# Kernel tuning notes

Measured on AMD Instinct MI355X. Metric: run time of the kernel, lower is better.

The kernel has to match this reference:

```python
import jax, jax.numpy as jnp
import numpy as np
from jax.scipy.special import logsumexp

B, D, T, O = 8, 64, 512, 256  # batch, channels (d_dim), observed timestamps, grid points


def setup_inputs() -> dict:
    key = jax.random.key(0)
    k1, k2, k3 = jax.random.split(key, 3)
    vals = jax.random.normal(k1, (B, D, T), dtype=jnp.float32)
    mask = (jax.random.uniform(k2, (B, D, T)) < 0.7).astype(jnp.float32)
    mask = mask.at[:, :, 0].set(1.0)  # ensure >=1 observation per (b, channel)
    times = jnp.sort(jax.random.uniform(k3, (B, D, T), dtype=jnp.float32), axis=-1)
    x = jnp.concatenate([vals, mask, times], axis=1)  # (B, 3*D, T)
    grid = jnp.broadcast_to(jnp.linspace(0.0, 1.0, O, dtype=jnp.float32), (B, O))
    kernel = jnp.zeros((D,), dtype=jnp.float32)  # learned per-channel log-bandwidth
    return {"x": x, "interpolation_grid": grid, "kernel": kernel}


def reference(x, interpolation_grid, kernel):
    d_dim = kernel.shape[0]
    x_t = x[:, :d_dim]            # (B, D, T) observed values
    m = x[:, d_dim:2 * d_dim]     # (B, D, T) observation mask in {0,1}
    t = x[:, 2 * d_dim:3 * d_dim] # (B, D, T) observation timestamps

    alpha = jax.nn.softplus(kernel)[None, :, None, None]  # pos_kernel, (1,D,1,1)
    # squared distance between observed times and reference grid: (B,D,T,O)
    norm = (t[:, :, :, None] - interpolation_grid[:, None, None, :]) ** 2
    # log(mask): -inf (clamped) where unobserved, 0 where observed
    logm = jnp.log(jnp.maximum(m, 1e-30))[:, :, :, None]

    s = -alpha * norm + logm                      # (B,D,T,O) masked RBF logits
    w = logsumexp(s, axis=2)                      # (B,D,O) intensity channel
    w1 = jnp.exp(s - w[:, :, None, :])            # softmax over T
    y = jnp.sum(w1 * x_t[:, :, :, None], axis=2)  # (B,D,O) smooth interpolation

    s10 = -10.0 * alpha * norm + logm             # sharper kernel (transient)
    wt_lse = logsumexp(s10, axis=2)
    wt = jnp.exp(s10 - wt_lse[:, :, None, :])
    y_trans = jnp.sum(wt * x_t[:, :, :, None], axis=2)  # (B,D,O)

    return jnp.concatenate([y, w, y_trans], axis=1)  # (B, 3*D, O)
```

## Files before the change

### kernel.cpp

```cpp
#include <hip/hip_runtime.h>
#include <math.h>


namespace {
constexpr int kB = 8, kD = 64, kT = 512, kO = 256;
constexpr float kLOG2E = 1.4426950408889634f;
constexpr float kLN2   = 0.6931471805599453f;
constexpr int kTH = 512;
}

__device__ __forceinline__ float rlane(float v, int l) {
    return __int_as_float(__builtin_amdgcn_readlane(__float_as_int(v), l));
}

__global__ __launch_bounds__(kTH, 4) void interp_kernel(
    const float* __restrict__ x,
    const float* __restrict__ grid,
    const float* __restrict__ kern,
    float* __restrict__ out)
{
    __shared__ float sp[4][4][kO];

    const int tid  = threadIdx.x;
    const int lane = tid & 63;
    const int wv   = tid >> 6;
    const int ow   = wv & 1;
    const int tw   = wv >> 1;
    const int o0   = ow * 128 + lane;
    const int t0   = tw * 128;

    const int bd = blockIdx.x;
    const int b  = bd >> 6;
    const int d  = bd & (kD - 1);

    const float* base = x + (size_t)b * (3 * kD * kT);
    const float* Vrow = base + (size_t)d * kT;
    const float* Mrow = base + (size_t)(kD + d) * kT;
    const float* Trow = base + (size_t)(2 * kD + d) * kT;

    const float k     = kern[d];
    const float alpha = fmaxf(k, 0.0f) + log1pf(expf(-fabsf(k)));
    const float a2    = alpha * kLOG2E;

    const float tt0 = Trow[t0 + lane],      tt1 = Trow[t0 + 64 + lane];
    const float mm0 = Mrow[t0 + lane],      mm1 = Mrow[t0 + 64 + lane];
    const float vv0 = Vrow[t0 + lane],      vv1 = Vrow[t0 + 64 + lane];
    const float lm0 = __builtin_amdgcn_logf(fmaxf(mm0, 1e-30f));
    const float lm1 = __builtin_amdgcn_logf(fmaxf(mm1, 1e-30f));
    const float u0  = fmaf(-a2 * tt0, tt0, lm0);
    const float u1  = fmaf(-a2 * tt1, tt1, lm1);
    const float w0  = 2.0f * a2 * tt0;
    const float w1  = 2.0f * a2 * tt1;

    const float g0 = grid[b * kO + o0];
    const float g1 = grid[b * kO + o0 + 64];

    float l_0=0.f,l_1=0.f, y_0=0.f,y_1=0.f, q_0=0.f,q_1=0.f, z_0=0.f,z_1=0.f;

    #pragma unroll
    for (int j = 0; j < 64; ++j) {
        { const float us = rlane(u0, j), ws = rlane(w0, j), vs = rlane(vv0, j);
          const float a0 = ws * g0 + us;
          const float a1 = ws * g1 + us;
          const float e0 = __builtin_amdgcn_exp2f(a0);
          const float E0 = __builtin_amdgcn_exp2f(10.0f * a0);
          const float e1 = __builtin_amdgcn_exp2f(a1);
          const float E1 = __builtin_amdgcn_exp2f(10.0f * a1);
          l_0 += e0; y_0 = fmaf(e0, vs, y_0); q_0 += E0; z_0 = fmaf(E0, vs, z_0);
          l_1 += e1; y_1 = fmaf(e1, vs, y_1); q_1 += E1; z_1 = fmaf(E1, vs, z_1); }
        { const float us = rlane(u1, j), ws = rlane(w1, j), vs = rlane(vv1, j);
          const float a0 = ws * g0 + us;
          const float a1 = ws * g1 + us;
          const float e0 = __builtin_amdgcn_exp2f(a0);
          const float E0 = __builtin_amdgcn_exp2f(10.0f * a0);
          const float e1 = __builtin_amdgcn_exp2f(a1);
          const float E1 = __builtin_amdgcn_exp2f(10.0f * a1);
          l_0 += e0; y_0 = fmaf(e0, vs, y_0); q_0 += E0; z_0 = fmaf(E0, vs, z_0);
          l_1 += e1; y_1 = fmaf(e1, vs, y_1); q_1 += E1; z_1 = fmaf(E1, vs, z_1); }
    }

    sp[tw][0][o0] = l_0;  sp[tw][0][o0 + 64] = l_1;
    sp[tw][1][o0] = y_0;  sp[tw][1][o0 + 64] = y_1;
    sp[tw][2][o0] = q_0;  sp[tw][2][o0 + 64] = q_1;
    sp[tw][3][o0] = z_0;  sp[tw][3][o0 + 64] = z_1;
    __syncthreads();

    if (tw == 0) {
        float L0=0.f,L1=0.f, Y0=0.f,Y1=0.f, Q0=0.f,Q1=0.f, Z0=0.f,Z1=0.f;
        #pragma unroll
        for (int j = 0; j < 4; ++j) {
            L0 += sp[j][0][o0]; Y0 += sp[j][1][o0];
            Q0 += sp[j][2][o0]; Z0 += sp[j][3][o0];
            L1 += sp[j][0][o0 + 64]; Y1 += sp[j][1][o0 + 64];
            Q1 += sp[j][2][o0 + 64]; Z1 += sp[j][3][o0 + 64];
        }
        const float c0 = -a2 * g0 * g0;
        const float c1 = -a2 * g1 * g1;
        const float w0o = (__builtin_amdgcn_logf(L0) + c0) * kLN2;
        const float w1o = (__builtin_amdgcn_logf(L1) + c1) * kLN2;
        float* ob = out + (size_t)b * (3 * kD * kO);
        ob[(size_t)d * kO + o0]                 = Y0 / L0;
        ob[(size_t)d * kO + o0 + 64]            = Y1 / L1;
        ob[(size_t)(kD + d) * kO + o0]          = w0o;
        ob[(size_t)(kD + d) * kO + o0 + 64]     = w1o;
        ob[(size_t)(2 * kD + d) * kO + o0]      = Z0 / Q0;
        ob[(size_t)(2 * kD + d) * kO + o0 + 64] = Z1 / Q1;
    }
}

extern "C" void kernel_launch(void* const* d_in, const int* in_sizes, int n_in,
                              void* d_out, int out_size, void* d_ws, size_t ws_size,
                              hipStream_t stream) {
    const float* x    = (const float*)d_in[0];
    const float* grid = (const float*)d_in[1];
    const float* kern = (const float*)d_in[2];
    float* out        = (float*)d_out;
    interp_kernel<<<dim3(kB * kD), dim3(kTH), 0, stream>>>(x, grid, kern, out);
}
```

Before: 80.14 us.

## Stage per-timestamp coefficients in LDS and fold grid constant into exponent

Precomputed u, w and v per timestamp now go into shared memory and are read back as float4 vectors, replacing the per-iteration readlane broadcasts from registers. The -a2*g^2 term moves inside the exponent, which adds one op per element and makes the exponent relative to the true RBF distance. The log of the mask becomes a linear map (mask*kLM - kLM), avoiding a log instruction but assuming the mask is exactly 0 or 1. LDS reads replace the SALU/readlane path, while the exp-bound inner loop is left unchanged.

```diff
diff --git a/kernel.cpp b/kernel.cpp
--- a/kernel.cpp
+++ b/kernel.cpp
@@ -4,13 +4,10 @@
 
 namespace {
 constexpr int kB = 8, kD = 64, kT = 512, kO = 256;
+constexpr int kTH = 512;
 constexpr float kLOG2E = 1.4426950408889634f;
 constexpr float kLN2   = 0.6931471805599453f;
-constexpr int kTH = 512;
-}
-
-__device__ __forceinline__ float rlane(float v, int l) {
-    return __int_as_float(__builtin_amdgcn_readlane(__float_as_int(v), l));
+constexpr float kLM    = 99.65784284662087f;
 }
 
 __global__ __launch_bounds__(kTH, 4) void interp_kernel(
@@ -19,15 +16,18 @@
     const float* __restrict__ kern,
     float* __restrict__ out)
 {
-    __shared__ float sp[4][4][kO];
+    __shared__ __align__(16) float smem[4096];
+    float* s_u = smem;
+    float* s_w = smem + kT;
+    float* s_v = smem + 2 * kT;
 
     const int tid  = threadIdx.x;
     const int lane = tid & 63;
     const int wv   = tid >> 6;
     const int ow   = wv & 1;
-    const int tw   = wv >> 1;
+    const int tq   = wv >> 1;
     const int o0   = ow * 128 + lane;
-    const int t0   = tw * 128;
+    const int o1   = o0 + 64;
 
     const int bd = blockIdx.x;
     const int b  = bd >> 6;
@@ -42,69 +42,70 @@
     const float alpha = fmaxf(k, 0.0f) + log1pf(expf(-fabsf(k)));
     const float a2    = alpha * kLOG2E;
 
-    const float tt0 = Trow[t0 + lane],      tt1 = Trow[t0 + 64 + lane];
-    const float mm0 = Mrow[t0 + lane],      mm1 = Mrow[t0 + 64 + lane];
-    const float vv0 = Vrow[t0 + lane],      vv1 = Vrow[t0 + 64 + lane];
-    const float lm0 = __builtin_amdgcn_logf(fmaxf(mm0, 1e-30f));
-    const float lm1 = __builtin_amdgcn_logf(fmaxf(mm1, 1e-30f));
-    const float u0  = fmaf(-a2 * tt0, tt0, lm0);
-    const float u1  = fmaf(-a2 * tt1, tt1, lm1);
-    const float w0  = 2.0f * a2 * tt0;
-    const float w1  = 2.0f * a2 * tt1;
+    {
+        const float tt = Trow[tid];
+        const float mm = Mrow[tid];
+        const float lm = fmaf(mm, kLM, -kLM);
+        s_u[tid] = fmaf(-a2 * tt, tt, lm);
+        s_w[tid] = 2.0f * a2 * tt;
+        s_v[tid] = Vrow[tid];
+    }
+    __syncthreads();
 
     const float g0 = grid[b * kO + o0];
-    const float g1 = grid[b * kO + o0 + 64];
+    const float g1 = grid[b * kO + o1];
+    const float c0 = -a2 * g0 * g0;
+    const float c1 = -a2 * g1 * g1;
 
     float l_0=0.f,l_1=0.f, y_0=0.f,y_1=0.f, q_0=0.f,q_1=0.f, z_0=0.f,z_1=0.f;
 
-    #pragma unroll
-    for (int j = 0; j < 64; ++j) {
-        { const float us = rlane(u0, j), ws = rlane(w0, j), vs = rlane(vv0, j);
-          const float a0 = ws * g0 + us;
-          const float a1 = ws * g1 + us;
-          const float e0 = __builtin_amdgcn_exp2f(a0);
-          const float E0 = __builtin_amdgcn_exp2f(10.0f * a0);
-          const float e1 = __builtin_amdgcn_exp2f(a1);
-          const float E1 = __builtin_amdgcn_exp2f(10.0f * a1);
-          l_0 += e0; y_0 = fmaf(e0, vs, y_0); q_0 += E0; z_0 = fmaf(E0, vs, z_0);
-          l_1 += e1; y_1 = fmaf(e1, vs, y_1); q_1 += E1; z_1 = fmaf(E1, vs, z_1); }
-        { const float us = rlane(u1, j), ws = rlane(w1, j), vs = rlane(vv1, j);
-          const float a0 = ws * g0 + us;
-          const float a1 = ws * g1 + us;
-          const float e0 = __builtin_amdgcn_exp2f(a0);
-          const float E0 = __builtin_amdgcn_exp2f(10.0f * a0);
-          const float e1 = __builtin_amdgcn_exp2f(a1);
-          const float E1 = __builtin_amdgcn_exp2f(10.0f * a1);
-          l_0 += e0; y_0 = fmaf(e0, vs, y_0); q_0 += E0; z_0 = fmaf(E0, vs, z_0);
-          l_1 += e1; y_1 = fmaf(e1, vs, y_1); q_1 += E1; z_1 = fmaf(E1, vs, z_1); }
+    const int t0 = tq * 128;
+    #pragma unroll 2
+    for (int t = t0; t < t0 + 128; t += 4) {
+        const float4 uu = *(const float4*)(s_u + t);
+        const float4 ww = *(const float4*)(s_w + t);
+        const float4 vv = *(const float4*)(s_v + t);
+
+        #pragma unroll
+        for (int j = 0; j < 4; ++j) {
+            const float u = (&uu.x)[j], w = (&ww.x)[j], v = (&vv.x)[j];
+            const float a0 = fmaf(w, g0, u) + c0;
+            const float a1 = fmaf(w, g1, u) + c1;
+            const float e0 = __builtin_amdgcn_exp2f(a0);
+            const float E0 = __builtin_amdgcn_exp2f(10.0f * a0);
+            const float e1 = __builtin_amdgcn_exp2f(a1);
+            const float E1 = __builtin_amdgcn_exp2f(10.0f * a1);
+            l_0 += e0; y_0 = fmaf(e0, v, y_0); q_0 += E0; z_0 = fmaf(E0, v, z_0);
+            l_1 += e1; y_1 = fmaf(e1, v, y_1); q_1 += E1; z_1 = fmaf(E1, v, z_1);
+        }
     }
 
-    sp[tw][0][o0] = l_0;  sp[tw][0][o0 + 64] = l_1;
-    sp[tw][1][o0] = y_0;  sp[tw][1][o0 + 64] = y_1;
-    sp[tw][2][o0] = q_0;  sp[tw][2][o0 + 64] = q_1;
-    sp[tw][3][o0] = z_0;  sp[tw][3][o0 + 64] = z_1;
+    __syncthreads();
+    float (*sp)[4][kO] = (float (*)[4][kO])smem;
+    sp[tq][0][o0] = l_0;  sp[tq][0][o1] = l_1;
+    sp[tq][1][o0] = y_0;  sp[tq][1][o1] = y_1;
+    sp[tq][2][o0] = q_0;  sp[tq][2][o1] = q_1;
+    sp[tq][3][o0] = z_0;  sp[tq][3][o1] = z_1;
     __syncthreads();
 
-    if (tw == 0) {
+    if (tq == 0) {
         float L0=0.f,L1=0.f, Y0=0.f,Y1=0.f, Q0=0.f,Q1=0.f, Z0=0.f,Z1=0.f;
         #pragma unroll
         for (int j = 0; j < 4; ++j) {
             L0 += sp[j][0][o0]; Y0 += sp[j][1][o0];
             Q0 += sp[j][2][o0]; Z0 += sp[j][3][o0];
-            L1 += sp[j][0][o0 + 64]; Y1 += sp[j][1][o0 + 64];
-            Q1 += sp[j][2][o0 + 64]; Z1 += sp[j][3][o0 + 64];
+            L1 += sp[j][0][o1]; Y1 += sp[j][1][o1];
+            Q1 += sp[j][2][o1]; Z1 += sp[j][3][o1];
         }
-        const float c0 = -a2 * g0 * g0;
-        const float c1 = -a2 * g1 * g1;
-        const float w0o = (__builtin_amdgcn_logf(L0) + c0) * kLN2;
-        const float w1o = (__builtin_amdgcn_logf(L1) + c1) * kLN2;
+        const float w0o = __builtin_amdgcn_logf(L0) * kLN2;
+        const float w1o = __builtin_amdgcn_logf(L1) * kLN2;
         float* ob = out + (size_t)b * (3 * kD * kO);
-        ob[(size_t)d * kO + o0]                 = Y0 / L0;
-        ob[(size_t)d * kO + o0 + 64]            = Y1 / L1;
-        ob[(size_t)(kD + d) * kO + o0]          = w0o;
-        ob[(size_t)(kD + d) * kO + o0 + 64]     = w1o;
-        ob[(size_t)(2 * kD + d) * kO + o0]      = Z0 / Q0;
-        ob[(size_t)(2 * kD + d) * kO + o0 + 64] = Z1 / Q1;
+        ob[(size_t)d * kO + o0]            = Y0 / L0;
+        ob[(size_t)d * kO + o1]            = Y1 / L1;
+        ob[(size_t)(kD + d) * kO + o0]     = w0o;
+        ob[(size_t)(kD + d) * kO + o1]     = w1o;
+        ob[(size_t)(2 * kD + d) * kO + o0] = Z0 / Q0;
+        ob[(size_t)(2 * kD + d) * kO + o1] = Z1 / Q1;
     }
 }
 
```

After: 76.18 us. -4.9%, faster.
